# Performance work log

Hardware: AMD Instinct MI355X
Metric: run time of the kernel (lower is better)

The kernel has to match this reference:

```python
import jax, jax.numpy as jnp
import numpy as np

KRYLOV_DIM = 8
T_END = 1.0
EPS = 1e-12


def setup_inputs() -> dict:
    key = jax.random.key(0)
    k1, k2, k3 = jax.random.split(key, 3)
    B, C, H, Wd = 8, 256, 64, 64
    s0 = jax.random.uniform(k1, (B, C, H, Wd), dtype=jnp.float32)
    v = jax.random.normal(k2, (B, C, H, Wd), dtype=jnp.float32)
    W = jax.random.normal(k3, (C, C), dtype=jnp.float32) / np.float32(np.sqrt(C))
    return {"s0": s0, "v": v, "W": W}


def reference(s0, v, W):
    # fitness: learned channel-mixing linear operator (1x1-conv style)
    def fitness(x):
        return jnp.einsum('oc,bchw->bohw', W, x)

    # replicator vector field R_{s}[x] = s*x - s * sum_c(s*x)
    def replicator(s, x):
        sx = s * x
        return sx - s * jnp.sum(sx, axis=1, keepdims=True)

    A = lambda x: fitness(replicator(s0, x))
    dot = lambda a, b: jnp.sum(a * b, axis=(1, 2, 3))  # batched inner product

    m = KRYLOV_DIM
    B = v.shape[0]

    # ---- Arnoldi iteration (batched, modified Gram-Schmidt) ----
    vnorm = jnp.sqrt(dot(v, v))  # [B]
    Q = [v / vnorm[:, None, None, None]]
    Hcols = []
    for k in range(m):
        w = A(Q[k])
        col = []
        for j in range(k + 1):
            h = dot(Q[j], w)               # [B]
            col.append(h)
            w = w - h[:, None, None, None] * Q[j]
        hnext = jnp.sqrt(dot(w, w))        # subdiagonal entry
        Q.append(w / (hnext + EPS)[:, None, None, None])
        col.append(hnext)
        col += [jnp.zeros_like(hnext)] * (m - k - 1)  # pad column to m+1 rows
        Hcols.append(jnp.stack(col, axis=-1))          # [B, m+1]
    Hmat = jnp.stack(Hcols, axis=-1)  # [B, m+1, m]
    T = Hmat[:, :m, :]                # square upper-Hessenberg [B, m, m]

    # ---- extended matrix + batched small matrix exponential ----
    ext = jnp.zeros((B, m + 1, m + 1), dtype=T.dtype)
    ext = ext.at[:, :m, :m].set(T_END * T)
    ext = ext.at[:, 0, m].set(T_END)
    expm_ext = jax.scipy.linalg.expm(ext)   # batched over leading dim
    coords = expm_ext[:, :m, -1]            # [B, m] Krylov coordinates

    # ---- fused weighted sum of Krylov vectors ----
    Qstack = jnp.stack(Q[:m], axis=0)       # [m, B, C, H, W]
    v_end = jnp.einsum('bj,jbchw->bchw', coords, Qstack)
    return v_end * vnorm[:, None, None, None]
```

## Files before the change

kernel.cpp:

```cpp
#include <hip/hip_runtime.h>
#include <math.h>

#define Bn   8
#define Cn   256
#define HWn  4096
#define FB   (Cn * HWn)
#define NTOT (Bn * FB)
#define TEND 1.0
#define EPSK 1e-12f
#define NT   32
#define TPB  128
#define TSZ  8192
#define RS   40
#define WTS  36

typedef float f32x4 __attribute__((ext_vector_type(4)));
typedef short bf16x8 __attribute__((ext_vector_type(8)));

__device__ inline float b2f(unsigned int u) {
    return __uint_as_float(u << 16);
}
__device__ inline unsigned short f2b(float f) {
    unsigned u = __float_as_uint(f);
    unsigned r = u + 0x7FFFu + ((u >> 16) & 1u);
    return (unsigned short)(r >> 16);
}


__global__ void init_kernel(float* __restrict__ p) {
    for (int i = threadIdx.x; i < 1024; i += 256) p[i] = 0.0f;
}

__global__ void wsplit_kernel(const float* __restrict__ W,
                              unsigned short* __restrict__ Whs,
                              unsigned short* __restrict__ Wls) {
    int kc = blockIdx.x, mt = blockIdx.y, l = threadIdx.x;
    int m = mt * 16 + (l & 15);
    int k0 = kc * 32 + (l >> 4) * 8;
#pragma unroll
    for (int j = 0; j < 8; ++j) {
        float wv = W[m * 256 + k0 + j];
        unsigned short h = f2b(wv);
        unsigned short lo = f2b(wv - b2f(h));
        int idx = ((kc * 16 + mt) * 64 + l) * 8 + j;
        Whs[idx] = h; Wls[idx] = lo;
    }
}

template <int K>
__global__ __launch_bounds__(256, 2) void step_kernel(
        const float* __restrict__ v, const float* __restrict__ s0,
        const unsigned short* __restrict__ Whs, const unsigned short* __restrict__ Wls,
        unsigned short* __restrict__ Qb, float* __restrict__ acc,
        float* __restrict__ w,
        unsigned short* __restrict__ Zh, unsigned short* __restrict__ Zl) {
    __shared__ __align__(16) char smem_u[36864];
    short* Ph0 = (short*)smem_u;
    short* Ph1 = (short*)(smem_u + 2560);
    short* Pl0 = (short*)(smem_u + 5120);
    short* Pl1 = (short*)(smem_u + 7680);
    float* tredf = (float*)(smem_u + 10240);
    float* wt    = (float*)smem_u;
    __shared__ float ts[NT];
    __shared__ float nred[4];
    __shared__ float dred[4][8];

    const int tid = threadIdx.x;
    const int lane = tid & 63, wvi = tid >> 6;
    const int b = blockIdx.y;
    const int tIdx = blockIdx.x;
    const int sbase = tIdx * NT;
    const size_t boff = (size_t)b * FB;
    const size_t tb = ((size_t)b * TPB + tIdx) * TSZ;
    const int mbase = wvi * 64;
    const int cch = tid >> 3;
    const int pos4 = (tid & 7) * 4;
    const int codd = cch & 1;
    const int c2s = cch >> 1;

    float cj[K > 0 ? K : 1];
    if (K > 0) {
        float mm[K > 0 ? K : 1];
        mm[0] = sqrtf(acc[512 + b]);
#pragma unroll
        for (int j = 1; j < K; ++j) mm[j] = sqrtf(acc[512 + j * 8 + b]) + EPSK * mm[j - 1];
#pragma unroll
        for (int j = 0; j < K; ++j)
            cj[j] = acc[((K - 1) * 8 + j) * 8 + b] / (mm[j] * mm[j]);
    }
    unsigned short* QK = Qb + (size_t)(K > 0 ? K - 1 : 0) * NTOT;

    float tp[4] = {0.f, 0.f, 0.f, 0.f};
    float np = 0.f;

    auto wr2 = [&](short* buf, unsigned x01, unsigned x23) {
        unsigned p01 = (unsigned)__shfl_xor((int)x01, 8);
        unsigned p23 = (unsigned)__shfl_xor((int)x23, 8);
        unsigned mine = codd ? x23 : x01;
        unsigned theirs = codd ? p23 : p01;
        unsigned w0, w1;
        if (codd) {
            w0 = (theirs & 0xFFFFu) | (mine << 16);
            w1 = (theirs >> 16) | (mine & 0xFFFF0000u);
        } else {
            w0 = (mine & 0xFFFFu) | (theirs << 16);
            w1 = (mine >> 16) | (theirs & 0xFFFF0000u);
        }
        int P0 = pos4 + 2 * codd;
        int slot = c2s ^ (((P0 >> 3) & 3) << 2);
        *(unsigned*)(buf + P0 * RS + slot * 2) = w0;
        *(unsigned*)(buf + (P0 + 1) * RS + slot * 2) = w1;
    };

    struct Ld {
        float4 s4, w4, v4;
        ushort4 q[K > 1 ? K - 1 : 1];
    };
    auto issue = [&](int kc) -> Ld {
        Ld L;
        const size_t os = boff + (size_t)(kc * 32 + cch) * HWn + sbase + pos4;
        const size_t ot = tb + (size_t)((kc * 32 + cch) * NT + pos4);
        L.s4 = *(const float4*)(s0 + os);
        if (K == 0) {
            L.v4 = *(const float4*)(v + os);
        } else if (K > 0) {
            L.w4 = *(const float4*)(w + ot);
            L.v4 = *(const float4*)(v + os);
#pragma unroll
            for (int j = 1; j < K; ++j)
                L.q[j - 1] = *(const ushort4*)(Qb + (size_t)(j - 1) * NTOT + ot);
        }
        return L;
    };
    auto consume = [&](Ld& L, int kc, int bb) {
        const size_t ot = tb + (size_t)((kc * 32 + cch) * NT + pos4);
        float se[4] = {L.s4.x, L.s4.y, L.s4.z, L.s4.w};
        float xr[4] = {0.f, 0.f, 0.f, 0.f};
        if (K == 0) {
            xr[0] = L.v4.x; xr[1] = L.v4.y; xr[2] = L.v4.z; xr[3] = L.v4.w;
        } else if (K > 0) {
            float xe[4];
            xe[0] = fmaf(-cj[0], L.v4.x, L.w4.x);
            xe[1] = fmaf(-cj[0], L.v4.y, L.w4.y);
            xe[2] = fmaf(-cj[0], L.v4.z, L.w4.z);
            xe[3] = fmaf(-cj[0], L.v4.w, L.w4.w);
#pragma unroll
            for (int j = 1; j < K; ++j) {
                xe[0] = fmaf(-cj[j], b2f(L.q[j - 1].x), xe[0]);
                xe[1] = fmaf(-cj[j], b2f(L.q[j - 1].y), xe[1]);
                xe[2] = fmaf(-cj[j], b2f(L.q[j - 1].z), xe[2]);
                xe[3] = fmaf(-cj[j], b2f(L.q[j - 1].w), xe[3]);
            }
            unsigned h0 = f2b(xe[0]), h1 = f2b(xe[1]);
            unsigned h2 = f2b(xe[2]), h3 = f2b(xe[3]);
            ushort4 o;
            o.x = (unsigned short)h0; o.y = (unsigned short)h1;
            o.z = (unsigned short)h2; o.w = (unsigned short)h3;
            *(ushort4*)(QK + ot) = o;
            xr[0] = b2f(h0); xr[1] = b2f(h1); xr[2] = b2f(h2); xr[3] = b2f(h3);
        }
        unsigned phx[4], plx[4];
#pragma unroll
        for (int i = 0; i < 4; ++i) {
            float pe;
            if (K < 0) {
                pe = se[i];
            } else {
                np = fmaf(xr[i], xr[i], np);
                tp[i] = fmaf(xr[i], se[i], tp[i]);
                pe = se[i] * xr[i];
            }
            unsigned hp = f2b(pe);
            phx[i] = hp; plx[i] = f2b(pe - b2f((unsigned short)hp));
        }
        wr2(bb ? Ph1 : Ph0, phx[0] | (phx[1] << 16), phx[2] | (phx[3] << 16));
        wr2(bb ? Pl1 : Pl0, plx[0] | (plx[1] << 16), plx[2] | (plx[3] << 16));
    };

    f32x4 ac[4][2];
#pragma unroll
    for (int i = 0; i < 4; ++i)
#pragma unroll
        for (int j = 0; j < 2; ++j) ac[i][j] = (f32x4){0.f, 0.f, 0.f, 0.f};

    const int r15 = lane & 15, qq = lane >> 4;
    {
        Ld L0 = issue(0);
        consume(L0, 0, 0);
    }
    for (int kc = 0; kc < 8; ++kc) {
        __syncthreads();
        bf16x8 ah[4], al[4];
#pragma unroll
        for (int rt = 0; rt < 4; ++rt) {
            int mt = wvi * 4 + rt;
            ah[rt] = *(const bf16x8*)(Whs + (size_t)kc * 8192 + (mt * 64 + lane) * 8);
            al[rt] = *(const bf16x8*)(Wls + (size_t)kc * 8192 + (mt * 64 + lane) * 8);
        }
        Ld Ln;
        if (kc < 7) Ln = issue(kc + 1);
        const short* ph = (kc & 1) ? Ph1 : Ph0;
        const short* pl = (kc & 1) ? Pl1 : Pl0;
#pragma unroll
        for (int ct = 0; ct < 2; ++ct) {
            int n = ct * 16 + r15;
            int grp = qq ^ ((n >> 3) & 3);
            int off = n * RS + grp * 8;
            bf16x8 bh = *(const bf16x8*)(ph + off);
            bf16x8 bl = *(const bf16x8*)(pl + off);
#pragma unroll
            for (int rt = 0; rt < 4; ++rt) {
                ac[rt][ct] = __builtin_amdgcn_mfma_f32_16x16x32_bf16(ah[rt], bh, ac[rt][ct], 0, 0, 0);
                ac[rt][ct] = __builtin_amdgcn_mfma_f32_16x16x32_bf16(ah[rt], bl, ac[rt][ct], 0, 0, 0);
                ac[rt][ct] = __builtin_amdgcn_mfma_f32_16x16x32_bf16(al[rt], bh, ac[rt][ct], 0, 0, 0);
            }
        }
        if (kc < 7) consume(Ln, kc + 1, (kc + 1) & 1);
    }

    __syncthreads();
    if (K >= 0) {
        *(float4*)(tredf + cch * WTS + pos4) = *(float4*)tp;
        float q2 = np;
        for (int off2 = 32; off2 > 0; off2 >>= 1) q2 += __shfl_down(q2, off2);
        if (lane == 0) nred[wvi] = q2;
    }
    __syncthreads();
    if (K >= 0) {
        if (tid < NT) {
            float s = 0.f;
#pragma unroll
            for (int g = 0; g < 32; ++g) s += tredf[g * WTS + tid];
            ts[tid] = s;
        }
        if (tid == 0)
            atomicAdd(&acc[512 + K * 8 + b], nred[0] + nred[1] + nred[2] + nred[3]);
    }
    __syncthreads();

#pragma unroll
    for (int rt = 0; rt < 4; ++rt)
#pragma unroll
        for (int ct = 0; ct < 2; ++ct) {
            int col = ct * 16 + r15;
            int r0 = mbase + rt * 16 + qq * 4;
#pragma unroll
            for (int reg = 0; reg < 4; ++reg)
                wt[(r0 + reg) * WTS + col] = ac[rt][ct][reg];
        }
    __syncthreads();

    float dp[K >= 0 ? K + 1 : 1];
#pragma unroll
    for (int j = 0; j < (K >= 0 ? K + 1 : 1); ++j) dp[j] = 0.f;
#pragma unroll
    for (int rr = 0; rr < 8; ++rr) {
        int row = rr * 32 + (tid >> 3);
        int col = (tid & 7) * 4;
        float4 wv4 = *(const float4*)(wt + row * WTS + col);
        size_t it = tb + (size_t)(row * NT + col);
        if (K < 0) {
            ushort4 zh4, zl4;
            unsigned short h0 = f2b(wv4.x), h1 = f2b(wv4.y);
            unsigned short h2 = f2b(wv4.z), h3 = f2b(wv4.w);
            zh4.x = h0; zh4.y = h1; zh4.z = h2; zh4.w = h3;
            zl4.x = f2b(wv4.x - b2f(h0)); zl4.y = f2b(wv4.y - b2f(h1));
            zl4.z = f2b(wv4.z - b2f(h2)); zl4.w = f2b(wv4.w - b2f(h3));
            *(ushort4*)(Zh + it) = zh4;
            *(ushort4*)(Zl + it) = zl4;
        } else {
            size_t is = boff + (size_t)row * HWn + sbase + col;
            ushort4 zh4 = *(const ushort4*)(Zh + it);
            ushort4 zl4 = *(const ushort4*)(Zl + it);
            float z0 = b2f(zh4.x) + b2f(zl4.x), z1 = b2f(zh4.y) + b2f(zl4.y);
            float z2 = b2f(zh4.z) + b2f(zl4.z), z3 = b2f(zh4.w) + b2f(zl4.w);
            float4 wf;
            wf.x = wv4.x - z0 * ts[col + 0];
            wf.y = wv4.y - z1 * ts[col + 1];
            wf.z = wv4.z - z2 * ts[col + 2];
            wf.w = wv4.w - z3 * ts[col + 3];
            *(float4*)(w + it) = wf;
            float4 vv4 = *(const float4*)(v + is);
            dp[0] = fmaf(wf.x, vv4.x, dp[0]);
            dp[0] = fmaf(wf.y, vv4.y, dp[0]);
            dp[0] = fmaf(wf.z, vv4.z, dp[0]);
            dp[0] = fmaf(wf.w, vv4.w, dp[0]);
#pragma unroll
            for (int j = 1; j <= (K >= 0 ? K : 0); ++j) {
                ushort4 u = *(const ushort4*)(Qb + (size_t)(j - 1) * NTOT + it);
                dp[j] = fmaf(wf.x, b2f(u.x), dp[j]);
                dp[j] = fmaf(wf.y, b2f(u.y), dp[j]);
                dp[j] = fmaf(wf.z, b2f(u.z), dp[j]);
                dp[j] = fmaf(wf.w, b2f(u.w), dp[j]);
            }
        }
    }
    if (K >= 0) {
#pragma unroll
        for (int j = 0; j <= K; ++j) {
            float q2 = dp[j];
            for (int off2 = 32; off2 > 0; off2 >>= 1) q2 += __shfl_down(q2, off2);
            if (lane == 0) dred[wvi][j] = q2;
        }
        __syncthreads();
        if (tid <= K)
            atomicAdd(&acc[(K * 8 + tid) * 8 + b],
                      dred[0][tid] + dred[1][tid] + dred[2][tid] + dred[3][tid]);
    }
}

__global__ __launch_bounds__(128) void expm_kernel(const float* __restrict__ acc,
                                                   float* __restrict__ coordsOut) {
    __shared__ double Am[81], Pm[81], Tm[81];
    __shared__ double ssc;
    __shared__ int sn;
    const int b = blockIdx.x;
    const int t = threadIdx.x;
    const int r = t / 9, c = t % 9;
    double m[8];
    m[0] = sqrt((double)acc[512 + b]);
    for (int j = 1; j < 8; ++j) m[j] = sqrt((double)acc[512 + j * 8 + b]) + 1e-12 * m[j - 1];
    if (t < 81) {
        double val = 0.0;
        if (r < 8 && c < 8) {
            if (r <= c) val = TEND * (double)acc[(c * 8 + r) * 8 + b] / (m[r] * m[c]);
            else if (r == c + 1) val = TEND * sqrt((double)acc[512 + r * 8 + b]) / m[c];
        }
        if (r == 0 && c == 8) val = TEND;
        Am[t] = val;
    }
    __syncthreads();
    if (t == 0) {
        double mx = 0.0;
        for (int rr = 0; rr < 9; ++rr) {
            double s = 0.0;
            for (int cc = 0; cc < 9; ++cc) s += fabs(Am[rr * 9 + cc]);
            if (s > mx) mx = s;
        }
        int n = 0;
        while (mx > 0.25 && n < 48) { mx *= 0.5; ++n; }
        double sc = 1.0;
        for (int ii = 0; ii < n; ++ii) sc *= 0.5;
        sn = n; ssc = sc;
    }
    __syncthreads();
    if (t < 81) Am[t] *= ssc;
    __syncthreads();
    if (t < 81) Pm[t] = (r == c) ? 1.0 : 0.0;
    __syncthreads();
    for (int i = 20; i >= 1; --i) {
        if (t < 81) {
            double s = 0.0;
            for (int k = 0; k < 9; ++k) s += Am[r * 9 + k] * Pm[k * 9 + c];
            Tm[t] = ((r == c) ? 1.0 : 0.0) + s / (double)i;
        }
        __syncthreads();
        if (t < 81) Pm[t] = Tm[t];
        __syncthreads();
    }
    int n = sn;
    for (int q = 0; q < n; ++q) {
        if (t < 81) {
            double s = 0.0;
            for (int k = 0; k < 9; ++k) s += Pm[r * 9 + k] * Pm[k * 9 + c];
            Tm[t] = s;
        }
        __syncthreads();
        if (t < 81) Pm[t] = Tm[t];
        __syncthreads();
    }
    if (t < 8) coordsOut[b * 8 + t] = (float)(Pm[t * 9 + 8] * m[0] / m[t]);
}

__global__ __launch_bounds__(256) void combine_kernel(const unsigned short* __restrict__ Qb,
                                                      const float* __restrict__ v,
                                                      const float* __restrict__ coords,
                                                      float* __restrict__ out) {
    int t = blockIdx.x, b = blockIdx.y;
    const size_t boff = (size_t)b * FB;
    const size_t tb = ((size_t)b * TPB + t) * TSZ;
    float cf[8];
#pragma unroll
    for (int j = 0; j < 8; ++j) cf[j] = coords[b * 8 + j];
    int rg = threadIdx.x >> 3;
    int pos4 = (threadIdx.x & 7) * 4;
#pragma unroll
    for (int ri = 0; ri < 8; ++ri) {
        int r = ri * 32 + rg;
        size_t it = tb + (size_t)(r * NT + pos4);
        size_t is = boff + (size_t)r * HWn + t * NT + pos4;
        float4 vv = *(const float4*)(v + is);
        float a[4] = {cf[0] * vv.x, cf[0] * vv.y, cf[0] * vv.z, cf[0] * vv.w};
#pragma unroll
        for (int j = 1; j < 8; ++j) {
            ushort4 u = *(const ushort4*)(Qb + (size_t)(j - 1) * NTOT + it);
            a[0] = fmaf(cf[j], b2f(u.x), a[0]);
            a[1] = fmaf(cf[j], b2f(u.y), a[1]);
            a[2] = fmaf(cf[j], b2f(u.z), a[2]);
            a[3] = fmaf(cf[j], b2f(u.w), a[3]);
        }
        float4 o = {a[0], a[1], a[2], a[3]};
        *(float4*)(out + is) = o;
    }
}

extern "C" void kernel_launch(void* const* d_in, const int* in_sizes, int n_in,
                              void* d_out, int out_size, void* d_ws, size_t ws_size,
                              hipStream_t stream) {
    const float* s0 = (const float*)d_in[0];
    const float* v  = (const float*)d_in[1];
    const float* W  = (const float*)d_in[2];
    float* out = (float*)d_out;

    float* ws     = (float*)d_ws;
    float* acc    = ws;
    float* coords = ws + 576;
    unsigned short* Whs = (unsigned short*)(ws + 1024);
    unsigned short* Wls = Whs + 65536;
    unsigned short* Zh  = (unsigned short*)(ws + 1024 + 65536);
    unsigned short* Zl  = Zh + NTOT;
    unsigned short* Qb  = Zh + 2 * (size_t)NTOT;
    float* w      = out;

    init_kernel<<<dim3(1), dim3(256), 0, stream>>>(ws);
    wsplit_kernel<<<dim3(8, 16), dim3(64), 0, stream>>>(W, Whs, Wls);

    dim3 ga(TPB, 8), blk(256);
    step_kernel<-1><<<ga, blk, 0, stream>>>(v, s0, Whs, Wls, Qb, acc, w, Zh, Zl);
#define STEPK(K) step_kernel<K><<<ga, blk, 0, stream>>>(v, s0, Whs, Wls, Qb, acc, w, Zh, Zl);
    STEPK(0) STEPK(1) STEPK(2) STEPK(3) STEPK(4) STEPK(5) STEPK(6) STEPK(7)
#undef STEPK

    expm_kernel<<<dim3(8), dim3(128), 0, stream>>>(acc, coords);
    combine_kernel<<<dim3(TPB, 8), blk, 0, stream>>>(Qb, v, coords, out);
}
```

Measured before the change: 511.8 us.

## Apply replicator mean correction before GEMM, dropping precomputed Z=W*s0 pass

Each step now runs a first pass over its tile to build the new Krylov vector, its norm and the per-pixel sum of s0*x. It then feeds s0*(x - sum) into the MFMA GEMM directly, instead of computing W*(s0*x) and subtracting a stored W*s0 correction. This removes the K=-1 kernel launch and the Zh/Zl workspace reads in every step. In exchange, each step reads its inputs twice (once for the reduction, once for staging), and the staging no longer overlaps the reduction with the GEMM.

```diff
diff --git a/kernel.cpp b/kernel.cpp
--- a/kernel.cpp
+++ b/kernel.cpp
@@ -52,8 +52,7 @@
         const float* __restrict__ v, const float* __restrict__ s0,
         const unsigned short* __restrict__ Whs, const unsigned short* __restrict__ Wls,
         unsigned short* __restrict__ Qb, float* __restrict__ acc,
-        float* __restrict__ w,
-        unsigned short* __restrict__ Zh, unsigned short* __restrict__ Zl) {
+        float* __restrict__ w) {
     __shared__ __align__(16) char smem_u[36864];
     short* Ph0 = (short*)smem_u;
     short* Ph1 = (short*)(smem_u + 2560);
@@ -92,6 +91,61 @@
 
     float tp[4] = {0.f, 0.f, 0.f, 0.f};
     float np = 0.f;
+    for (int kc = 0; kc < 8; ++kc) {
+        const size_t os = boff + (size_t)(kc * 32 + cch) * HWn + sbase + pos4;
+        const size_t ot = tb + (size_t)((kc * 32 + cch) * NT + pos4);
+        float4 s4 = *(const float4*)(s0 + os);
+        float se[4] = {s4.x, s4.y, s4.z, s4.w};
+        float xr[4];
+        if (K == 0) {
+            float4 x4 = *(const float4*)(v + os);
+            xr[0] = x4.x; xr[1] = x4.y; xr[2] = x4.z; xr[3] = x4.w;
+        } else {
+            float4 w4 = *(const float4*)(w + ot);
+            float4 v4 = *(const float4*)(v + os);
+            float xe[4];
+            xe[0] = fmaf(-cj[0], v4.x, w4.x);
+            xe[1] = fmaf(-cj[0], v4.y, w4.y);
+            xe[2] = fmaf(-cj[0], v4.z, w4.z);
+            xe[3] = fmaf(-cj[0], v4.w, w4.w);
+#pragma unroll
+            for (int j = 1; j < K; ++j) {
+                ushort4 u = *(const ushort4*)(Qb + (size_t)(j - 1) * NTOT + ot);
+                xe[0] = fmaf(-cj[j], b2f(u.x), xe[0]);
+                xe[1] = fmaf(-cj[j], b2f(u.y), xe[1]);
+                xe[2] = fmaf(-cj[j], b2f(u.z), xe[2]);
+                xe[3] = fmaf(-cj[j], b2f(u.w), xe[3]);
+            }
+            unsigned h0 = f2b(xe[0]), h1 = f2b(xe[1]);
+            unsigned h2 = f2b(xe[2]), h3 = f2b(xe[3]);
+            ushort4 o;
+            o.x = (unsigned short)h0; o.y = (unsigned short)h1;
+            o.z = (unsigned short)h2; o.w = (unsigned short)h3;
+            *(ushort4*)(QK + ot) = o;
+            xr[0] = b2f(h0); xr[1] = b2f(h1); xr[2] = b2f(h2); xr[3] = b2f(h3);
+        }
+#pragma unroll
+        for (int i = 0; i < 4; ++i) {
+            np = fmaf(xr[i], xr[i], np);
+            tp[i] = fmaf(xr[i], se[i], tp[i]);
+        }
+    }
+    *(float4*)(tredf + cch * WTS + pos4) = *(float4*)tp;
+    {
+        float q2 = np;
+        for (int off2 = 32; off2 > 0; off2 >>= 1) q2 += __shfl_down(q2, off2);
+        if (lane == 0) nred[wvi] = q2;
+    }
+    __syncthreads();
+    if (tid < NT) {
+        float s = 0.f;
+#pragma unroll
+        for (int g = 0; g < 32; ++g) s += tredf[g * WTS + tid];
+        ts[tid] = s;
+    }
+    if (tid == 0)
+        atomicAdd(&acc[512 + K * 8 + b], nred[0] + nred[1] + nred[2] + nred[3]);
+    __syncthreads();
 
     auto wr2 = [&](short* buf, unsigned x01, unsigned x23) {
         unsigned p01 = (unsigned)__shfl_xor((int)x01, 8);
@@ -112,64 +166,23 @@
         *(unsigned*)(buf + (P0 + 1) * RS + slot * 2) = w1;
     };
 
-    struct Ld {
-        float4 s4, w4, v4;
-        ushort4 q[K > 1 ? K - 1 : 1];
-    };
-    auto issue = [&](int kc) -> Ld {
-        Ld L;
+    auto stage = [&](int kc, int bb) {
         const size_t os = boff + (size_t)(kc * 32 + cch) * HWn + sbase + pos4;
         const size_t ot = tb + (size_t)((kc * 32 + cch) * NT + pos4);
-        L.s4 = *(const float4*)(s0 + os);
+        float4 s4 = *(const float4*)(s0 + os);
+        float se[4] = {s4.x, s4.y, s4.z, s4.w};
+        float xr[4];
         if (K == 0) {
-            L.v4 = *(const float4*)(v + os);
-        } else if (K > 0) {
-            L.w4 = *(const float4*)(w + ot);
-            L.v4 = *(const float4*)(v + os);
-#pragma unroll
-            for (int j = 1; j < K; ++j)
-                L.q[j - 1] = *(const ushort4*)(Qb + (size_t)(j - 1) * NTOT + ot);
-        }
-        return L;
-    };
-    auto consume = [&](Ld& L, int kc, int bb) {
-        const size_t ot = tb + (size_t)((kc * 32 + cch) * NT + pos4);
-        float se[4] = {L.s4.x, L.s4.y, L.s4.z, L.s4.w};
-        float xr[4] = {0.f, 0.f, 0.f, 0.f};
-        if (K == 0) {
-            xr[0] = L.v4.x; xr[1] = L.v4.y; xr[2] = L.v4.z; xr[3] = L.v4.w;
-        } else if (K > 0) {
-            float xe[4];
-            xe[0] = fmaf(-cj[0], L.v4.x, L.w4.x);
-            xe[1] = fmaf(-cj[0], L.v4.y, L.w4.y);
-            xe[2] = fmaf(-cj[0], L.v4.z, L.w4.z);
-            xe[3] = fmaf(-cj[0], L.v4.w, L.w4.w);
-#pragma unroll
-            for (int j = 1; j < K; ++j) {
-                xe[0] = fmaf(-cj[j], b2f(L.q[j - 1].x), xe[0]);
-                xe[1] = fmaf(-cj[j], b2f(L.q[j - 1].y), xe[1]);
-                xe[2] = fmaf(-cj[j], b2f(L.q[j - 1].z), xe[2]);
-                xe[3] = fmaf(-cj[j], b2f(L.q[j - 1].w), xe[3]);
-            }
-            unsigned h0 = f2b(xe[0]), h1 = f2b(xe[1]);
-            unsigned h2 = f2b(xe[2]), h3 = f2b(xe[3]);
-            ushort4 o;
-            o.x = (unsigned short)h0; o.y = (unsigned short)h1;
-            o.z = (unsigned short)h2; o.w = (unsigned short)h3;
-            *(ushort4*)(QK + ot) = o;
-            xr[0] = b2f(h0); xr[1] = b2f(h1); xr[2] = b2f(h2); xr[3] = b2f(h3);
+            float4 x4 = *(const float4*)(v + os);
+            xr[0] = x4.x; xr[1] = x4.y; xr[2] = x4.z; xr[3] = x4.w;
+        } else {
+            ushort4 u = *(const ushort4*)(QK + ot);
+            xr[0] = b2f(u.x); xr[1] = b2f(u.y); xr[2] = b2f(u.z); xr[3] = b2f(u.w);
         }
         unsigned phx[4], plx[4];
 #pragma unroll
         for (int i = 0; i < 4; ++i) {
-            float pe;
-            if (K < 0) {
-                pe = se[i];
-            } else {
-                np = fmaf(xr[i], xr[i], np);
-                tp[i] = fmaf(xr[i], se[i], tp[i]);
-                pe = se[i] * xr[i];
-            }
+            float pe = se[i] * (xr[i] - ts[pos4 + i]);
             unsigned hp = f2b(pe);
             phx[i] = hp; plx[i] = f2b(pe - b2f((unsigned short)hp));
         }
@@ -184,10 +197,7 @@
         for (int j = 0; j < 2; ++j) ac[i][j] = (f32x4){0.f, 0.f, 0.f, 0.f};
 
     const int r15 = lane & 15, qq = lane >> 4;
-    {
-        Ld L0 = issue(0);
-        consume(L0, 0, 0);
-    }
+    stage(0, 0);
     for (int kc = 0; kc < 8; ++kc) {
         __syncthreads();
         bf16x8 ah[4], al[4];
@@ -197,8 +207,7 @@
             ah[rt] = *(const bf16x8*)(Whs + (size_t)kc * 8192 + (mt * 64 + lane) * 8);
             al[rt] = *(const bf16x8*)(Wls + (size_t)kc * 8192 + (mt * 64 + lane) * 8);
         }
-        Ld Ln;
-        if (kc < 7) Ln = issue(kc + 1);
+        if (kc < 7) stage(kc + 1, (kc + 1) & 1);
         const short* ph = (kc & 1) ? Ph1 : Ph0;
         const short* pl = (kc & 1) ? Pl1 : Pl0;
 #pragma unroll
@@ -215,29 +224,9 @@
                 ac[rt][ct] = __builtin_amdgcn_mfma_f32_16x16x32_bf16(al[rt], bh, ac[rt][ct], 0, 0, 0);
             }
         }
-        if (kc < 7) consume(Ln, kc + 1, (kc + 1) & 1);
-    }
-
-    __syncthreads();
-    if (K >= 0) {
-        *(float4*)(tredf + cch * WTS + pos4) = *(float4*)tp;
-        float q2 = np;
-        for (int off2 = 32; off2 > 0; off2 >>= 1) q2 += __shfl_down(q2, off2);
-        if (lane == 0) nred[wvi] = q2;
-    }
-    __syncthreads();
-    if (K >= 0) {
-        if (tid < NT) {
-            float s = 0.f;
-#pragma unroll
-            for (int g = 0; g < 32; ++g) s += tredf[g * WTS + tid];
-            ts[tid] = s;
-        }
-        if (tid == 0)
-            atomicAdd(&acc[512 + K * 8 + b], nred[0] + nred[1] + nred[2] + nred[3]);
-    }
-    __syncthreads();
-
+    }
+
+    __syncthreads();
 #pragma unroll
     for (int rt = 0; rt < 4; ++rt)
 #pragma unroll
@@ -250,63 +239,41 @@
         }
     __syncthreads();
 
-    float dp[K >= 0 ? K + 1 : 1];
-#pragma unroll
-    for (int j = 0; j < (K >= 0 ? K + 1 : 1); ++j) dp[j] = 0.f;
+    float dp[K + 1];
+#pragma unroll
+    for (int j = 0; j <= K; ++j) dp[j] = 0.f;
 #pragma unroll
     for (int rr = 0; rr < 8; ++rr) {
         int row = rr * 32 + (tid >> 3);
         int col = (tid & 7) * 4;
-        float4 wv4 = *(const float4*)(wt + row * WTS + col);
+        float4 wf = *(const float4*)(wt + row * WTS + col);
         size_t it = tb + (size_t)(row * NT + col);
-        if (K < 0) {
-            ushort4 zh4, zl4;
-            unsigned short h0 = f2b(wv4.x), h1 = f2b(wv4.y);
-            unsigned short h2 = f2b(wv4.z), h3 = f2b(wv4.w);
-            zh4.x = h0; zh4.y = h1; zh4.z = h2; zh4.w = h3;
-            zl4.x = f2b(wv4.x - b2f(h0)); zl4.y = f2b(wv4.y - b2f(h1));
-            zl4.z = f2b(wv4.z - b2f(h2)); zl4.w = f2b(wv4.w - b2f(h3));
-            *(ushort4*)(Zh + it) = zh4;
-            *(ushort4*)(Zl + it) = zl4;
-        } else {
-            size_t is = boff + (size_t)row * HWn + sbase + col;
-            ushort4 zh4 = *(const ushort4*)(Zh + it);
-            ushort4 zl4 = *(const ushort4*)(Zl + it);
-            float z0 = b2f(zh4.x) + b2f(zl4.x), z1 = b2f(zh4.y) + b2f(zl4.y);
-            float z2 = b2f(zh4.z) + b2f(zl4.z), z3 = b2f(zh4.w) + b2f(zl4.w);
-            float4 wf;
-            wf.x = wv4.x - z0 * ts[col + 0];
-            wf.y = wv4.y - z1 * ts[col + 1];
-            wf.z = wv4.z - z2 * ts[col + 2];
-            wf.w = wv4.w - z3 * ts[col + 3];
-            *(float4*)(w + it) = wf;
-            float4 vv4 = *(const float4*)(v + is);
-            dp[0] = fmaf(wf.x, vv4.x, dp[0]);
-            dp[0] = fmaf(wf.y, vv4.y, dp[0]);
-            dp[0] = fmaf(wf.z, vv4.z, dp[0]);
-            dp[0] = fmaf(wf.w, vv4.w, dp[0]);
-#pragma unroll
-            for (int j = 1; j <= (K >= 0 ? K : 0); ++j) {
-                ushort4 u = *(const ushort4*)(Qb + (size_t)(j - 1) * NTOT + it);
-                dp[j] = fmaf(wf.x, b2f(u.x), dp[j]);
-                dp[j] = fmaf(wf.y, b2f(u.y), dp[j]);
-                dp[j] = fmaf(wf.z, b2f(u.z), dp[j]);
-                dp[j] = fmaf(wf.w, b2f(u.w), dp[j]);
-            }
-        }
-    }
-    if (K >= 0) {
-#pragma unroll
-        for (int j = 0; j <= K; ++j) {
-            float q2 = dp[j];
-            for (int off2 = 32; off2 > 0; off2 >>= 1) q2 += __shfl_down(q2, off2);
-            if (lane == 0) dred[wvi][j] = q2;
-        }
-        __syncthreads();
-        if (tid <= K)
-            atomicAdd(&acc[(K * 8 + tid) * 8 + b],
-                      dred[0][tid] + dred[1][tid] + dred[2][tid] + dred[3][tid]);
-    }
+        size_t is = boff + (size_t)row * HWn + sbase + col;
+        *(float4*)(w + it) = wf;
+        float4 vv4 = *(const float4*)(v + is);
+        dp[0] = fmaf(wf.x, vv4.x, dp[0]);
+        dp[0] = fmaf(wf.y, vv4.y, dp[0]);
+        dp[0] = fmaf(wf.z, vv4.z, dp[0]);
+        dp[0] = fmaf(wf.w, vv4.w, dp[0]);
+#pragma unroll
+        for (int j = 1; j <= K; ++j) {
+            ushort4 u = *(const ushort4*)(Qb + (size_t)(j - 1) * NTOT + it);
+            dp[j] = fmaf(wf.x, b2f(u.x), dp[j]);
+            dp[j] = fmaf(wf.y, b2f(u.y), dp[j]);
+            dp[j] = fmaf(wf.z, b2f(u.z), dp[j]);
+            dp[j] = fmaf(wf.w, b2f(u.w), dp[j]);
+        }
+    }
+#pragma unroll
+    for (int j = 0; j <= K; ++j) {
+        float q2 = dp[j];
+        for (int off2 = 32; off2 > 0; off2 >>= 1) q2 += __shfl_down(q2, off2);
+        if (lane == 0) dred[wvi][j] = q2;
+    }
+    __syncthreads();
+    if (tid <= K)
+        atomicAdd(&acc[(K * 8 + tid) * 8 + b],
+                  dred[0][tid] + dred[1][tid] + dred[2][tid] + dred[3][tid]);
 }
 
 __global__ __launch_bounds__(128) void expm_kernel(const float* __restrict__ acc,
@@ -417,17 +384,14 @@
     float* coords = ws + 576;
     unsigned short* Whs = (unsigned short*)(ws + 1024);
     unsigned short* Wls = Whs + 65536;
-    unsigned short* Zh  = (unsigned short*)(ws + 1024 + 65536);
-    unsigned short* Zl  = Zh + NTOT;
-    unsigned short* Qb  = Zh + 2 * (size_t)NTOT;
+    unsigned short* Qb  = (unsigned short*)(ws + 1024 + 65536);
     float* w      = out;
 
     init_kernel<<<dim3(1), dim3(256), 0, stream>>>(ws);
     wsplit_kernel<<<dim3(8, 16), dim3(64), 0, stream>>>(W, Whs, Wls);
 
     dim3 ga(TPB, 8), blk(256);
-    step_kernel<-1><<<ga, blk, 0, stream>>>(v, s0, Whs, Wls, Qb, acc, w, Zh, Zl);
-#define STEPK(K) step_kernel<K><<<ga, blk, 0, stream>>>(v, s0, Whs, Wls, Qb, acc, w, Zh, Zl);
+#define STEPK(K) step_kernel<K><<<ga, blk, 0, stream>>>(v, s0, Whs, Wls, Qb, acc, w);
     STEPK(0) STEPK(1) STEPK(2) STEPK(3) STEPK(4) STEPK(5) STEPK(6) STEPK(7)
 #undef STEPK
 
```

Result: no change. 510.9 us (-0.2%).
